# Performance work log

Hardware: AMD Instinct MI355X
Metric: run time of the kernel (lower is better)

## Reference

```python
import jax, jax.numpy as jnp
import numpy as np

DT_SCALER = 1.0 / 24.0
ODE_STEPS = 4  # fixed-step RK4 stand-in for adaptive odeint(rtol=atol=1e-3)
B, T, D, H = 1024, 100, 32, 256
ODE_MID = 50  # hidden width of the ODE func MLP (hard-coded 50 in source)


def setup_inputs() -> dict:
    key = jax.random.key(0)
    ks = jax.random.split(key, 20)
    n = lambda k, s: jax.random.normal(k, s, dtype=jnp.float32)
    std = 0.1  # module inits weights N(0, 0.1), biases 0
    return {
        "dt": jax.random.uniform(ks[0], (B, T, 2), dtype=jnp.float32),
        "x": n(ks[1], (B, T, D)),
        # RNNCell params
        "W_ih": n(ks[2], (H, D)) * std,
        "b_ih": jnp.zeros((H,), jnp.float32),
        "W_hh": n(ks[3], (H, H)) * std,
        "b_hh": jnp.zeros((H,), jnp.float32),
        # ODE func: Linear(H,50) -> tanh -> Linear(50,H)
        "ode_w1": n(ks[4], (ODE_MID, H)) * std,
        "ode_b1": jnp.zeros((ODE_MID,), jnp.float32),
        "ode_w2": n(ks[5], (H, ODE_MID)) * std,
        "ode_b2": jnp.zeros((H,), jnp.float32),
        # mu head: l1 (H -> H//2), distribution_mu (H//2 -> 1)
        "l1_w": n(ks[6], (H // 2, H)) * std,
        "l1_b": jnp.zeros((H // 2,), jnp.float32),
        "mu_w": n(ks[7], (1, H // 2)) * std,
        "mu_b": jnp.zeros((1,), jnp.float32),
        # sigma head: Linear(H,H) -> tanh -> Linear(H,1) -> softplus
        "sig_w1": n(ks[8], (H, H)) * std,
        "sig_b1": jnp.zeros((H,), jnp.float32),
        "sig_w2": n(ks[9], (1, H)) * std,
        "sig_b2": jnp.zeros((1,), jnp.float32),
    }


def reference(dt, x, W_ih, b_ih, W_hh, b_hh, ode_w1, ode_b1, ode_w2, ode_b2,
              l1_w, l1_b, mu_w, mu_b, sig_w1, sig_b1, sig_w2, sig_b2):
    Bsz = x.shape[0]
    xs = jnp.swapaxes(x, 0, 1)                               # [T,B,D]
    dts = jnp.swapaxes(dt[:, :, 1] - dt[:, :, 0], 0, 1)[..., None]  # [T,B,1]
    h0 = jnp.zeros((Bsz, W_hh.shape[0]), x.dtype)
    hs = 1.0 / ODE_STEPS

    def ode_f(y, scale):
        # net(y) * (dt * DT_SCALER); RHS is time-independent
        return (jnp.tanh(y @ ode_w1.T + ode_b1) @ ode_w2.T + ode_b2) * scale

    def step(h, inp):
        x_i, dt_i = inp                                      # [B,D], [B,1]
        # h_t = h_t + RNNCell(x_i, h_t)
        h = h + jnp.tanh(x_i @ W_ih.T + b_ih + h @ W_hh.T + b_hh)
        scale = dt_i * DT_SCALER
        # integrate dh/dt = ode_f(h) from t=0 to t=1 (fixed-step RK4)
        def rk4(y, _):
            k1 = ode_f(y, scale)
            k2 = ode_f(y + 0.5 * hs * k1, scale)
            k3 = ode_f(y + 0.5 * hs * k2, scale)
            k4 = ode_f(y + hs * k3, scale)
            return y + (hs / 6.0) * (k1 + 2.0 * k2 + 2.0 * k3 + k4), None
        h, _ = jax.lax.scan(rk4, h, None, length=ODE_STEPS)
        # heads (eval mode: dropout is identity)
        mu = jax.nn.relu(h @ l1_w.T + l1_b) @ mu_w.T + mu_b              # [B,1]
        sig = jax.nn.softplus(jnp.tanh(h @ sig_w1.T + sig_b1) @ sig_w2.T + sig_b2)
        return h, (mu, sig)

    _, (mu_seq, sig_seq) = jax.lax.scan(step, h0, (xs, dts))
    mu_out = jnp.swapaxes(mu_seq, 0, 1)    # [B,T,1]
    sig_out = jnp.swapaxes(sig_seq, 0, 1)  # [B,T,1]
    return (mu_out, sig_out)
```

## Files before the change

### kernel.cpp

```cpp
#include <hip/hip_runtime.h>
#include <math.h>


#define NT 512

#define WS_WCAT 0
#define WS_L1P  73728
#define WS_SW1  106496
#define WS_TOT  172032

#define SM_PR1 0
#define SM_PR2 10240
#define SM_H   20480
#define SM_YC  21504
#define SM_AC  22528
#define SM_MD  23552
#define SM_X4  23808
#define SM_BC  23936
#define SM_OB1 24192
#define SM_OB2 24256
#define SM_L1B 24512
#define SM_SB1 24640
#define SM_MUW 24896
#define SM_SW2 25024
#define SM_SCL 25280
#define SM_TOT 25288
#define SMEM_BYTES (SM_TOT * 4)

__device__ __forceinline__ float fma4(float acc, float4 y, float4 w) {
  acc = fmaf(y.x, w.x, acc);
  acc = fmaf(y.y, w.y, acc);
  acc = fmaf(y.z, w.z, acc);
  acc = fmaf(y.w, w.w, acc);
  return acc;
}

__device__ __forceinline__ float4 add4(float4 a, float4 b) {
  return make_float4(a.x + b.x, a.y + b.y, a.z + b.z, a.w + b.w);
}

__device__ __forceinline__ float tfast(float x) {
  float ax = fabsf(x);
  float e  = __expf(-2.f * ax);
  float t  = (1.f - e) * __builtin_amdgcn_rcpf(1.f + e);
  return copysignf(t, x);
}

__device__ __forceinline__ float4 tfast4(float4 v) {
  return make_float4(tfast(v.x), tfast(v.y), tfast(v.z), tfast(v.w));
}

__global__ void prep_transpose(const float* __restrict__ Wih,
                               const float* __restrict__ Whh,
                               const float* __restrict__ l1w,
                               const float* __restrict__ sw1,
                               float* __restrict__ ws) {
  int i = blockIdx.x * 256 + threadIdx.x;
  if (i < 73728) {
    int g = i >> 10, rem = i & 1023, j = rem >> 2, c = rem & 3;
    int k = 4 * g + c;
    ws[i] = (k < 32) ? Wih[j * 32 + k] : Whh[j * 256 + (k - 32)];
  } else if (i < 106496) {
    int t = i - 73728;
    int g = t >> 9, rem = t & 511, j = rem >> 2, c = rem & 3;
    ws[i] = l1w[j * 256 + 4 * g + c];
  } else if (i < WS_TOT) {
    int t = i - 106496;
    int g = t >> 10, rem = t & 1023, j = rem >> 2, c = rem & 3;
    ws[i] = sw1[j * 256 + 4 * g + c];
  }
}

__global__ __attribute__((amdgpu_flat_work_group_size(NT, NT)))
__attribute__((amdgpu_waves_per_eu(2)))
void odernn_main(const float* __restrict__ dt,
                 const float* __restrict__ x,
                 const float* __restrict__ bih,
                 const float* __restrict__ bhh,
                 const float* __restrict__ ow1,
                 const float* __restrict__ ob1g,
                 const float* __restrict__ ow2,
                 const float* __restrict__ ob2g,
                 const float* __restrict__ l1bg,
                 const float* __restrict__ muwg,
                 const float* __restrict__ mubg,
                 const float* __restrict__ sb1g,
                 const float* __restrict__ sw2g,
                 const float* __restrict__ sb2g,
                 const float* __restrict__ ws,
                 float* __restrict__ out) {
  extern __shared__ __align__(16) float sm[];
  const int tid = threadIdx.x;
  const int wv = tid >> 6, ln = tid & 63;
  const int b0 = blockIdx.x * 4;

  float* prS  = sm + SM_PR1;
  float* prS2 = sm + SM_PR2;
  float* hS   = sm + SM_H;
  float* ycS  = sm + SM_YC;
  float* acS  = sm + SM_AC;
  float* mdS  = sm + SM_MD;
  float* x4S  = sm + SM_X4;
  float* bcS  = sm + SM_BC;
  float* ob1S = sm + SM_OB1;
  float* ob2S = sm + SM_OB2;
  float* l1bS = sm + SM_L1B;
  float* sb1S = sm + SM_SB1;
  float* muwS = sm + SM_MUW;
  float* sw2S = sm + SM_SW2;
  float* sclS = sm + SM_SCL;

  float4* pr1_4 = (float4*)prS;
  float4* pr2_4 = (float4*)prS2;
  float4* h4   = (float4*)hS;
  float4* yc4  = (float4*)ycS;
  float4* ac4  = (float4*)acS;
  float4* md4w = (float4*)mdS;
  float4* l1o4 = (float4*)ycS;
  float4* sg4  = (float4*)acS;
  const float4* h44  = (const float4*)hS;
  const float4* yc44 = (const float4*)ycS;
  const float4* md4  = (const float4*)mdS;
  const float4* x44  = (const float4*)x4S;
  const float4* bc4  = (const float4*)bcS;
  const float4* ob1_4 = (const float4*)ob1S;
  const float4* ob2_4 = (const float4*)ob2S;
  const float4* l1b4 = (const float4*)l1bS;
  const float4* sb14 = (const float4*)sb1S;
  const float4* muw4 = (const float4*)muwS;
  const float4* sw24 = (const float4*)sw2S;

  const float4* wcat4 = (const float4*)(ws + WS_WCAT);
  const float4* l1w4  = (const float4*)(ws + WS_L1P);
  const float4* sw14  = (const float4*)(ws + WS_SW1);

  const int q1 = tid & 15, kc1 = tid >> 4;
  const int cq2 = tid & 63, kc2 = tid >> 6;
  float4 w1r[4][2];
  float4 w2r[4][2];
  {
#pragma unroll
    for (int n = 0; n < 4; ++n) {
      int row = 4 * q1 + n;
#pragma unroll
      for (int g = 0; g < 2; ++g) {
        if (row < 50)
          w1r[n][g] = *(const float4*)&ow1[row * 256 + kc1 * 8 + 4 * g];
        else
          w1r[n][g] = make_float4(0.f, 0.f, 0.f, 0.f);
      }
    }
    float w2tmp[4];
#pragma unroll
    for (int n = 0; n < 4; ++n) {
      int col = 4 * cq2 + n;
#pragma unroll
      for (int g = 0; g < 2; ++g) {
#pragma unroll
        for (int c = 0; c < 4; ++c) {
          int k = kc2 * 8 + 4 * g + c;
          w2tmp[c] = (k < 50) ? ow2[col * 50 + k] : 0.f;
        }
        w2r[n][g] = make_float4(w2tmp[0], w2tmp[1], w2tmp[2], w2tmp[3]);
      }
    }
  }

  if (tid < 256) {
    bcS[tid]  = bih[tid] + bhh[tid];
    ob2S[tid] = ob2g[tid];
    sb1S[tid] = sb1g[tid];
    sw2S[tid] = sw2g[tid];
  }
  if (tid < 64)  ob1S[tid] = (tid < 50) ? ob1g[tid] : 0.f;
  if (tid < 128) { l1bS[tid] = l1bg[tid]; muwS[tid] = muwg[tid]; }
  hS[tid] = 0.f; hS[tid + 512] = 0.f;
  __syncthreads();

  const float mub = mubg[0], sb2 = sb2g[0];

  for (int t = 0; t < 100; ++t) {
    if (tid < 128) {
      int r = tid >> 5, kk = tid & 31;
      x4S[r * 32 + kk] = x[((size_t)(b0 + r) * 100 + t) * 32 + kk];
    }
    if (tid < 4) {
      const float* dp = dt + ((size_t)(b0 + tid) * 100 + t) * 2;
      sclS[tid] = (dp[1] - dp[0]) * (1.f / 24.f);
    }
    __syncthreads();

    {
      const int jq = tid & 63, kc = tid >> 6;
      float4 acc0 = make_float4(0, 0, 0, 0), acc1 = acc0, acc2 = acc0, acc3 = acc0;
#pragma unroll 3
      for (int gg = 0; gg < 9; ++gg) {
        int g = kc * 9 + gg;
        float4 w0 = wcat4[g * 256 + 4 * jq + 0];
        float4 w1 = wcat4[g * 256 + 4 * jq + 1];
        float4 w2 = wcat4[g * 256 + 4 * jq + 2];
        float4 w3 = wcat4[g * 256 + 4 * jq + 3];
        float4 y0 = (g < 8) ? x44[0 * 8 + g] : h44[0 * 64 + (g - 8)];
        float4 y1 = (g < 8) ? x44[1 * 8 + g] : h44[1 * 64 + (g - 8)];
        float4 y2 = (g < 8) ? x44[2 * 8 + g] : h44[2 * 64 + (g - 8)];
        float4 y3 = (g < 8) ? x44[3 * 8 + g] : h44[3 * 64 + (g - 8)];
        acc0.x = fma4(acc0.x, y0, w0); acc0.y = fma4(acc0.y, y0, w1);
        acc0.z = fma4(acc0.z, y0, w2); acc0.w = fma4(acc0.w, y0, w3);
        acc1.x = fma4(acc1.x, y1, w0); acc1.y = fma4(acc1.y, y1, w1);
        acc1.z = fma4(acc1.z, y1, w2); acc1.w = fma4(acc1.w, y1, w3);
        acc2.x = fma4(acc2.x, y2, w0); acc2.y = fma4(acc2.y, y2, w1);
        acc2.z = fma4(acc2.z, y2, w2); acc2.w = fma4(acc2.w, y2, w3);
        acc3.x = fma4(acc3.x, y3, w0); acc3.y = fma4(acc3.y, y3, w1);
        acc3.z = fma4(acc3.z, y3, w2); acc3.w = fma4(acc3.w, y3, w3);
      }
      pr1_4[tid * 5 + 0] = acc0;
      pr1_4[tid * 5 + 1] = acc1;
      pr1_4[tid * 5 + 2] = acc2;
      pr1_4[tid * 5 + 3] = acc3;
    }
    __syncthreads();
    if (tid < 256) {
      const int r = tid >> 6, jq = tid & 63;
      const float4* base = pr1_4 + (jq * 5 + r);
      float4 v = base[0];
#pragma unroll
      for (int kc = 1; kc < 8; ++kc) v = add4(v, base[kc * 320]);
      v = add4(v, bc4[jq]);
      int o4 = r * 64 + jq;
      h4[o4] = add4(h4[o4], tfast4(v));
    }
    __syncthreads();

#pragma unroll 1
    for (int os = 0; os < 4; ++os) {
#pragma unroll
      for (int s = 0; s < 4; ++s) {
        {
          const float4* ysrc = (s == 0) ? h44 : yc44;
          float4 a0 = make_float4(0, 0, 0, 0), a1 = a0, a2 = a0, a3 = a0;
#pragma unroll
          for (int g = 0; g < 2; ++g) {
            float4 y0 = ysrc[0 * 64 + kc1 * 2 + g];
            float4 y1 = ysrc[1 * 64 + kc1 * 2 + g];
            float4 y2 = ysrc[2 * 64 + kc1 * 2 + g];
            float4 y3 = ysrc[3 * 64 + kc1 * 2 + g];
            a0.x = fma4(a0.x, y0, w1r[0][g]); a0.y = fma4(a0.y, y0, w1r[1][g]);
            a0.z = fma4(a0.z, y0, w1r[2][g]); a0.w = fma4(a0.w, y0, w1r[3][g]);
            a1.x = fma4(a1.x, y1, w1r[0][g]); a1.y = fma4(a1.y, y1, w1r[1][g]);
            a1.z = fma4(a1.z, y1, w1r[2][g]); a1.w = fma4(a1.w, y1, w1r[3][g]);
            a2.x = fma4(a2.x, y2, w1r[0][g]); a2.y = fma4(a2.y, y2, w1r[1][g]);
            a2.z = fma4(a2.z, y2, w1r[2][g]); a2.w = fma4(a2.w, y2, w1r[3][g]);
            a3.x = fma4(a3.x, y3, w1r[0][g]); a3.y = fma4(a3.y, y3, w1r[1][g]);
            a3.z = fma4(a3.z, y3, w1r[2][g]); a3.w = fma4(a3.w, y3, w1r[3][g]);
          }
          pr1_4[tid * 5 + 0] = a0;
          pr1_4[tid * 5 + 1] = a1;
          pr1_4[tid * 5 + 2] = a2;
          pr1_4[tid * 5 + 3] = a3;
        }
        __syncthreads();
        if (tid < 256) {
          const int r = tid >> 6, qr = (tid >> 2) & 15, sub = tid & 3;
          const float4* base = pr1_4 + ((sub * 16 + qr) * 5 + r);
          float4 v = base[0];
#pragma unroll
          for (int i = 1; i < 8; ++i) v = add4(v, base[i * 320]);
          v.x += __shfl_xor(v.x, 1); v.y += __shfl_xor(v.y, 1);
          v.z += __shfl_xor(v.z, 1); v.w += __shfl_xor(v.w, 1);
          v.x += __shfl_xor(v.x, 2); v.y += __shfl_xor(v.y, 2);
          v.z += __shfl_xor(v.z, 2); v.w += __shfl_xor(v.w, 2);
          if (sub == 0)
            md4w[r * 16 + qr] = tfast4(add4(v, ob1_4[qr]));
        }
        __syncthreads();
        {
          float4 b0v = make_float4(0, 0, 0, 0), b1v = b0v, b2v = b0v, b3v = b0v;
#pragma unroll
          for (int g = 0; g < 2; ++g) {
            float4 m0 = md4[0 * 16 + kc2 * 2 + g];
            float4 m1 = md4[1 * 16 + kc2 * 2 + g];
            float4 m2 = md4[2 * 16 + kc2 * 2 + g];
            float4 m3 = md4[3 * 16 + kc2 * 2 + g];
            b0v.x = fma4(b0v.x, m0, w2r[0][g]); b0v.y = fma4(b0v.y, m0, w2r[1][g]);
            b0v.z = fma4(b0v.z, m0, w2r[2][g]); b0v.w = fma4(b0v.w, m0, w2r[3][g]);
            b1v.x = fma4(b1v.x, m1, w2r[0][g]); b1v.y = fma4(b1v.y, m1, w2r[1][g]);
            b1v.z = fma4(b1v.z, m1, w2r[2][g]); b1v.w = fma4(b1v.w, m1, w2r[3][g]);
            b2v.x = fma4(b2v.x, m2, w2r[0][g]); b2v.y = fma4(b2v.y, m2, w2r[1][g]);
            b2v.z = fma4(b2v.z, m2, w2r[2][g]); b2v.w = fma4(b2v.w, m2, w2r[3][g]);
            b3v.x = fma4(b3v.x, m3, w2r[0][g]); b3v.y = fma4(b3v.y, m3, w2r[1][g]);
            b3v.z = fma4(b3v.z, m3, w2r[2][g]); b3v.w = fma4(b3v.w, m3, w2r[3][g]);
          }
          pr2_4[tid * 5 + 0] = b0v;
          pr2_4[tid * 5 + 1] = b1v;
          pr2_4[tid * 5 + 2] = b2v;
          pr2_4[tid * 5 + 3] = b3v;
        }
        __syncthreads();
        if (tid < 256) {
          const int r = tid >> 6, cq = tid & 63;
          const float4* base = pr2_4 + (cq * 5 + r);
          float4 v = base[0];
#pragma unroll
          for (int kc = 1; kc < 8; ++kc) v = add4(v, base[kc * 320]);
          v = add4(v, ob2_4[cq]);
          float sc = sclS[r];
          float4 kv = make_float4(v.x * sc, v.y * sc, v.z * sc, v.w * sc);
          int o4 = r * 64 + cq;
          if (s == 0) {
            ac4[o4] = kv;
            float4 hv = h4[o4];
            yc4[o4] = make_float4(hv.x + 0.125f * kv.x, hv.y + 0.125f * kv.y,
                                  hv.z + 0.125f * kv.z, hv.w + 0.125f * kv.w);
          } else if (s == 1) {
            float4 a = ac4[o4];
            ac4[o4] = make_float4(a.x + 2.f * kv.x, a.y + 2.f * kv.y,
                                  a.z + 2.f * kv.z, a.w + 2.f * kv.w);
            float4 hv = h4[o4];
            yc4[o4] = make_float4(hv.x + 0.125f * kv.x, hv.y + 0.125f * kv.y,
                                  hv.z + 0.125f * kv.z, hv.w + 0.125f * kv.w);
          } else if (s == 2) {
            float4 a = ac4[o4];
            ac4[o4] = make_float4(a.x + 2.f * kv.x, a.y + 2.f * kv.y,
                                  a.z + 2.f * kv.z, a.w + 2.f * kv.w);
            float4 hv = h4[o4];
            yc4[o4] = make_float4(hv.x + 0.25f * kv.x, hv.y + 0.25f * kv.y,
                                  hv.z + 0.25f * kv.z, hv.w + 0.25f * kv.w);
          } else {
            float4 a = ac4[o4];
            float4 hv = h4[o4];
            const float c6 = 0.25f / 6.f;
            h4[o4] = make_float4(hv.x + c6 * (a.x + kv.x), hv.y + c6 * (a.y + kv.y),
                                 hv.z + c6 * (a.z + kv.z), hv.w + c6 * (a.w + kv.w));
          }
        }
        __syncthreads();
      }
    }

    {
      const int cq = tid & 31, kc = tid >> 5;
      float4 c0 = make_float4(0, 0, 0, 0), c1 = c0, c2 = c0, c3 = c0;
#pragma unroll 2
      for (int g = 0; g < 4; ++g) {
        int kg = kc * 4 + g;
        float4 w0 = l1w4[kg * 128 + 4 * cq + 0];
        float4 w1 = l1w4[kg * 128 + 4 * cq + 1];
        float4 w2 = l1w4[kg * 128 + 4 * cq + 2];
        float4 w3 = l1w4[kg * 128 + 4 * cq + 3];
        float4 y0 = h44[0 * 64 + kg], y1 = h44[1 * 64 + kg];
        float4 y2 = h44[2 * 64 + kg], y3 = h44[3 * 64 + kg];
        c0.x = fma4(c0.x, y0, w0); c0.y = fma4(c0.y, y0, w1);
        c0.z = fma4(c0.z, y0, w2); c0.w = fma4(c0.w, y0, w3);
        c1.x = fma4(c1.x, y1, w0); c1.y = fma4(c1.y, y1, w1);
        c1.z = fma4(c1.z, y1, w2); c1.w = fma4(c1.w, y1, w3);
        c2.x = fma4(c2.x, y2, w0); c2.y = fma4(c2.y, y2, w1);
        c2.z = fma4(c2.z, y2, w2); c2.w = fma4(c2.w, y2, w3);
        c3.x = fma4(c3.x, y3, w0); c3.y = fma4(c3.y, y3, w1);
        c3.z = fma4(c3.z, y3, w2); c3.w = fma4(c3.w, y3, w3);
      }
      pr1_4[tid * 5 + 0] = c0;
      pr1_4[tid * 5 + 1] = c1;
      pr1_4[tid * 5 + 2] = c2;
      pr1_4[tid * 5 + 3] = c3;
    }
    {
      const int cq = tid & 63, kc = tid >> 6;
      float4 d0 = make_float4(0, 0, 0, 0), d1 = d0, d2 = d0, d3 = d0;
#pragma unroll 2
      for (int g = 0; g < 8; ++g) {
        int kg = kc * 8 + g;
        float4 w0 = sw14[kg * 256 + 4 * cq + 0];
        float4 w1 = sw14[kg * 256 + 4 * cq + 1];
        float4 w2 = sw14[kg * 256 + 4 * cq + 2];
        float4 w3 = sw14[kg * 256 + 4 * cq + 3];
        float4 y0 = h44[0 * 64 + kg], y1 = h44[1 * 64 + kg];
        float4 y2 = h44[2 * 64 + kg], y3 = h44[3 * 64 + kg];
        d0.x = fma4(d0.x, y0, w0); d0.y = fma4(d0.y, y0, w1);
        d0.z = fma4(d0.z, y0, w2); d0.w = fma4(d0.w, y0, w3);
        d1.x = fma4(d1.x, y1, w0); d1.y = fma4(d1.y, y1, w1);
        d1.z = fma4(d1.z, y1, w2); d1.w = fma4(d1.w, y1, w3);
        d2.x = fma4(d2.x, y2, w0); d2.y = fma4(d2.y, y2, w1);
        d2.z = fma4(d2.z, y2, w2); d2.w = fma4(d2.w, y2, w3);
        d3.x = fma4(d3.x, y3, w0); d3.y = fma4(d3.y, y3, w1);
        d3.z = fma4(d3.z, y3, w2); d3.w = fma4(d3.w, y3, w3);
      }
      pr2_4[tid * 5 + 0] = d0;
      pr2_4[tid * 5 + 1] = d1;
      pr2_4[tid * 5 + 2] = d2;
      pr2_4[tid * 5 + 3] = d3;
    }
    __syncthreads();
    if (tid < 256) {
      const int outQ = tid >> 1, sub = tid & 1;
      const int r = outQ >> 5, cq = outQ & 31;
      const float4* base = pr1_4 + ((sub * 32 + cq) * 5 + r);
      float4 v = base[0];
#pragma unroll
      for (int i = 1; i < 8; ++i) v = add4(v, base[i * 320]);
      v.x += __shfl_xor(v.x, 1); v.y += __shfl_xor(v.y, 1);
      v.z += __shfl_xor(v.z, 1); v.w += __shfl_xor(v.w, 1);
      if (sub == 0) {
        float4 b = l1b4[cq];
        l1o4[r * 32 + cq] = make_float4(fmaxf(v.x + b.x, 0.f), fmaxf(v.y + b.y, 0.f),
                                        fmaxf(v.z + b.z, 0.f), fmaxf(v.w + b.w, 0.f));
      }
    } else {
      const int t2 = tid & 255;
      const int r = t2 >> 6, cq = t2 & 63;
      const float4* base = pr2_4 + (cq * 5 + r);
      float4 v = base[0];
#pragma unroll
      for (int kc = 1; kc < 8; ++kc) v = add4(v, base[kc * 320]);
      sg4[r * 64 + cq] = tfast4(add4(v, sb14[cq]));
    }
    __syncthreads();
    {
      if (wv < 4) {
        const int r = wv, c = ln & 31;
        float4 l = l1o4[r * 32 + c], w = muw4[c];
        float pm = (ln < 32) ? (l.x * w.x + l.y * w.y + l.z * w.z + l.w * w.w) : 0.f;
#pragma unroll
        for (int off = 32; off > 0; off >>= 1) pm += __shfl_down(pm, off);
        if (ln == 0) out[(size_t)(b0 + r) * 100 + t] = pm + mub;
      } else {
        const int r = wv - 4;
        float4 s4 = sg4[r * 64 + ln], w = sw24[ln];
        float ps = s4.x * w.x + s4.y * w.y + s4.z * w.z + s4.w * w.w;
#pragma unroll
        for (int off = 32; off > 0; off >>= 1) ps += __shfl_down(ps, off);
        if (ln == 0) {
          float z = ps + sb2;
          float sp = fmaxf(z, 0.f) + log1pf(expf(-fabsf(z)));
          out[(size_t)102400 + (size_t)(b0 + r) * 100 + t] = sp;
        }
      }
    }
  }
}

extern "C" void kernel_launch(void* const* d_in, const int* in_sizes, int n_in,
                              void* d_out, int out_size, void* d_ws, size_t ws_size,
                              hipStream_t stream) {
  const float* dt  = (const float*)d_in[0];
  const float* x   = (const float*)d_in[1];
  const float* Wih = (const float*)d_in[2];
  const float* bih = (const float*)d_in[3];
  const float* Whh = (const float*)d_in[4];
  const float* bhh = (const float*)d_in[5];
  const float* ow1 = (const float*)d_in[6];
  const float* ob1 = (const float*)d_in[7];
  const float* ow2 = (const float*)d_in[8];
  const float* ob2 = (const float*)d_in[9];
  const float* l1w = (const float*)d_in[10];
  const float* l1b = (const float*)d_in[11];
  const float* muw = (const float*)d_in[12];
  const float* mub = (const float*)d_in[13];
  const float* sw1 = (const float*)d_in[14];
  const float* sb1 = (const float*)d_in[15];
  const float* sw2 = (const float*)d_in[16];
  const float* sb2 = (const float*)d_in[17];
  float* ws  = (float*)d_ws;
  float* out = (float*)d_out;

  hipFuncSetAttribute((const void*)odernn_main,
                      hipFuncAttributeMaxDynamicSharedMemorySize, SMEM_BYTES);

  prep_transpose<<<WS_TOT / 256, 256, 0, stream>>>(Wih, Whh, l1w, sw1, ws);
  odernn_main<<<256, NT, SMEM_BYTES, stream>>>(dt, x, bih, bhh, ow1, ob1, ow2, ob2,
                                               l1b, muw, mub, sb1, sw2, sb2, ws, out);
}
```

Measured before the change: 3.846 ms.

## Halve batch rows per block to double grid size and raise occupancy

Each workgroup now processes 2 batch rows instead of 4, so the grid grows from 256 to 512 blocks, filling more of the GPU's compute units. Partial-sum buffers are re-laid out into a single compact region with new reduction indexing and cross-lane shuffles, which shrinks LDS use, and the waves-per-EU hint rises to 4. The trade-off is that each weight load from global/L2 is now reused across only 2 rows instead of 4, doubling total weight traffic per step, and the recurrent time loop stays just as serial with the same number of barriers.

```diff
diff --git a/kernel.cpp b/kernel.cpp
--- a/kernel.cpp
+++ b/kernel.cpp
@@ -9,22 +9,21 @@
 #define WS_SW1  106496
 #define WS_TOT  172032
 
-#define SM_PR1 0
-#define SM_PR2 10240
-#define SM_H   20480
-#define SM_YC  21504
-#define SM_AC  22528
-#define SM_MD  23552
-#define SM_X4  23808
-#define SM_BC  23936
-#define SM_OB1 24192
-#define SM_OB2 24256
-#define SM_L1B 24512
-#define SM_SB1 24640
-#define SM_MUW 24896
-#define SM_SW2 25024
-#define SM_SCL 25280
-#define SM_TOT 25288
+#define SM_PR  0
+#define SM_H   8192
+#define SM_YC  8704
+#define SM_AC  9216
+#define SM_MD  9728
+#define SM_X4  9856
+#define SM_BC  9920
+#define SM_OB1 10176
+#define SM_OB2 10240
+#define SM_L1B 10496
+#define SM_SB1 10624
+#define SM_MUW 10880
+#define SM_SW2 11008
+#define SM_SCL 11264
+#define SM_TOT 11272
 #define SMEM_BYTES (SM_TOT * 4)
 
 __device__ __forceinline__ float fma4(float acc, float4 y, float4 w) {
@@ -72,7 +71,7 @@
 }
 
 __global__ __attribute__((amdgpu_flat_work_group_size(NT, NT)))
-__attribute__((amdgpu_waves_per_eu(2)))
+__attribute__((amdgpu_waves_per_eu(4)))
 void odernn_main(const float* __restrict__ dt,
                  const float* __restrict__ x,
                  const float* __restrict__ bih,
@@ -92,14 +91,9 @@
   extern __shared__ __align__(16) float sm[];
   const int tid = threadIdx.x;
   const int wv = tid >> 6, ln = tid & 63;
-  const int b0 = blockIdx.x * 4;
-
-  float* prS  = sm + SM_PR1;
-  float* prS2 = sm + SM_PR2;
+  const int b0 = blockIdx.x * 2;
+
   float* hS   = sm + SM_H;
-  float* ycS  = sm + SM_YC;
-  float* acS  = sm + SM_AC;
-  float* mdS  = sm + SM_MD;
   float* x4S  = sm + SM_X4;
   float* bcS  = sm + SM_BC;
   float* ob1S = sm + SM_OB1;
@@ -110,18 +104,17 @@
   float* sw2S = sm + SM_SW2;
   float* sclS = sm + SM_SCL;
 
-  float4* pr1_4 = (float4*)prS;
-  float4* pr2_4 = (float4*)prS2;
-  float4* h4   = (float4*)hS;
-  float4* yc4  = (float4*)ycS;
-  float4* ac4  = (float4*)acS;
-  float4* md4w = (float4*)mdS;
-  float4* l1o4 = (float4*)ycS;
-  float4* sg4  = (float4*)acS;
-  const float4* h44  = (const float4*)hS;
-  const float4* yc44 = (const float4*)ycS;
-  const float4* md4  = (const float4*)mdS;
-  const float4* x44  = (const float4*)x4S;
+  float4* pr4  = (float4*)(sm + SM_PR);
+  float4* h4   = (float4*)(sm + SM_H);
+  float4* yc4  = (float4*)(sm + SM_YC);
+  float4* ac4  = (float4*)(sm + SM_AC);
+  float4* md4w = (float4*)(sm + SM_MD);
+  float4* l1o4 = (float4*)(sm + SM_YC);
+  float4* sg4  = (float4*)(sm + SM_AC);
+  const float4* h44  = (const float4*)(sm + SM_H);
+  const float4* yc44 = (const float4*)(sm + SM_YC);
+  const float4* md4  = (const float4*)(sm + SM_MD);
+  const float4* x44  = (const float4*)(sm + SM_X4);
   const float4* bc4  = (const float4*)bcS;
   const float4* ob1_4 = (const float4*)ob1S;
   const float4* ob2_4 = (const float4*)ob2S;
@@ -174,17 +167,17 @@
   }
   if (tid < 64)  ob1S[tid] = (tid < 50) ? ob1g[tid] : 0.f;
   if (tid < 128) { l1bS[tid] = l1bg[tid]; muwS[tid] = muwg[tid]; }
-  hS[tid] = 0.f; hS[tid + 512] = 0.f;
+  if (tid < 512) hS[tid] = 0.f;
   __syncthreads();
 
   const float mub = mubg[0], sb2 = sb2g[0];
 
   for (int t = 0; t < 100; ++t) {
-    if (tid < 128) {
+    if (tid < 64) {
       int r = tid >> 5, kk = tid & 31;
       x4S[r * 32 + kk] = x[((size_t)(b0 + r) * 100 + t) * 32 + kk];
     }
-    if (tid < 4) {
+    if (tid < 2) {
       const float* dp = dt + ((size_t)(b0 + tid) * 100 + t) * 2;
       sclS[tid] = (dp[1] - dp[0]) * (1.f / 24.f);
     }
@@ -192,7 +185,7 @@
 
     {
       const int jq = tid & 63, kc = tid >> 6;
-      float4 acc0 = make_float4(0, 0, 0, 0), acc1 = acc0, acc2 = acc0, acc3 = acc0;
+      float4 acc0 = make_float4(0, 0, 0, 0), acc1 = acc0;
 #pragma unroll 3
       for (int gg = 0; gg < 9; ++gg) {
         int g = kc * 9 + gg;
@@ -200,31 +193,22 @@
         float4 w1 = wcat4[g * 256 + 4 * jq + 1];
         float4 w2 = wcat4[g * 256 + 4 * jq + 2];
         float4 w3 = wcat4[g * 256 + 4 * jq + 3];
-        float4 y0 = (g < 8) ? x44[0 * 8 + g] : h44[0 * 64 + (g - 8)];
-        float4 y1 = (g < 8) ? x44[1 * 8 + g] : h44[1 * 64 + (g - 8)];
-        float4 y2 = (g < 8) ? x44[2 * 8 + g] : h44[2 * 64 + (g - 8)];
-        float4 y3 = (g < 8) ? x44[3 * 8 + g] : h44[3 * 64 + (g - 8)];
+        float4 y0 = (g < 8) ? x44[g]     : h44[g - 8];
+        float4 y1 = (g < 8) ? x44[8 + g] : h44[64 + (g - 8)];
         acc0.x = fma4(acc0.x, y0, w0); acc0.y = fma4(acc0.y, y0, w1);
         acc0.z = fma4(acc0.z, y0, w2); acc0.w = fma4(acc0.w, y0, w3);
         acc1.x = fma4(acc1.x, y1, w0); acc1.y = fma4(acc1.y, y1, w1);
         acc1.z = fma4(acc1.z, y1, w2); acc1.w = fma4(acc1.w, y1, w3);
-        acc2.x = fma4(acc2.x, y2, w0); acc2.y = fma4(acc2.y, y2, w1);
-        acc2.z = fma4(acc2.z, y2, w2); acc2.w = fma4(acc2.w, y2, w3);
-        acc3.x = fma4(acc3.x, y3, w0); acc3.y = fma4(acc3.y, y3, w1);
-        acc3.z = fma4(acc3.z, y3, w2); acc3.w = fma4(acc3.w, y3, w3);
-      }
-      pr1_4[tid * 5 + 0] = acc0;
-      pr1_4[tid * 5 + 1] = acc1;
-      pr1_4[tid * 5 + 2] = acc2;
-      pr1_4[tid * 5 + 3] = acc3;
+      }
+      pr4[(kc * 2 + 0) * 64 + jq] = acc0;
+      pr4[(kc * 2 + 1) * 64 + jq] = acc1;
     }
     __syncthreads();
-    if (tid < 256) {
+    if (tid < 128) {
       const int r = tid >> 6, jq = tid & 63;
-      const float4* base = pr1_4 + (jq * 5 + r);
-      float4 v = base[0];
-#pragma unroll
-      for (int kc = 1; kc < 8; ++kc) v = add4(v, base[kc * 320]);
+      float4 v = pr4[r * 64 + jq];
+#pragma unroll
+      for (int kc = 1; kc < 8; ++kc) v = add4(v, pr4[(kc * 2 + r) * 64 + jq]);
       v = add4(v, bc4[jq]);
       int o4 = r * 64 + jq;
       h4[o4] = add4(h4[o4], tfast4(v));
@@ -237,71 +221,54 @@
       for (int s = 0; s < 4; ++s) {
         {
           const float4* ysrc = (s == 0) ? h44 : yc44;
-          float4 a0 = make_float4(0, 0, 0, 0), a1 = a0, a2 = a0, a3 = a0;
+          float4 a0 = make_float4(0, 0, 0, 0), a1 = a0;
 #pragma unroll
           for (int g = 0; g < 2; ++g) {
-            float4 y0 = ysrc[0 * 64 + kc1 * 2 + g];
-            float4 y1 = ysrc[1 * 64 + kc1 * 2 + g];
-            float4 y2 = ysrc[2 * 64 + kc1 * 2 + g];
-            float4 y3 = ysrc[3 * 64 + kc1 * 2 + g];
+            float4 y0 = ysrc[kc1 * 2 + g];
+            float4 y1 = ysrc[64 + kc1 * 2 + g];
             a0.x = fma4(a0.x, y0, w1r[0][g]); a0.y = fma4(a0.y, y0, w1r[1][g]);
             a0.z = fma4(a0.z, y0, w1r[2][g]); a0.w = fma4(a0.w, y0, w1r[3][g]);
             a1.x = fma4(a1.x, y1, w1r[0][g]); a1.y = fma4(a1.y, y1, w1r[1][g]);
             a1.z = fma4(a1.z, y1, w1r[2][g]); a1.w = fma4(a1.w, y1, w1r[3][g]);
-            a2.x = fma4(a2.x, y2, w1r[0][g]); a2.y = fma4(a2.y, y2, w1r[1][g]);
-            a2.z = fma4(a2.z, y2, w1r[2][g]); a2.w = fma4(a2.w, y2, w1r[3][g]);
-            a3.x = fma4(a3.x, y3, w1r[0][g]); a3.y = fma4(a3.y, y3, w1r[1][g]);
-            a3.z = fma4(a3.z, y3, w1r[2][g]); a3.w = fma4(a3.w, y3, w1r[3][g]);
           }
-          pr1_4[tid * 5 + 0] = a0;
-          pr1_4[tid * 5 + 1] = a1;
-          pr1_4[tid * 5 + 2] = a2;
-          pr1_4[tid * 5 + 3] = a3;
+          pr4[(kc1 * 2 + 0) * 16 + q1] = a0;
+          pr4[(kc1 * 2 + 1) * 16 + q1] = a1;
         }
         __syncthreads();
-        if (tid < 256) {
-          const int r = tid >> 6, qr = (tid >> 2) & 15, sub = tid & 3;
-          const float4* base = pr1_4 + ((sub * 16 + qr) * 5 + r);
-          float4 v = base[0];
-#pragma unroll
-          for (int i = 1; i < 8; ++i) v = add4(v, base[i * 320]);
-          v.x += __shfl_xor(v.x, 1); v.y += __shfl_xor(v.y, 1);
-          v.z += __shfl_xor(v.z, 1); v.w += __shfl_xor(v.w, 1);
-          v.x += __shfl_xor(v.x, 2); v.y += __shfl_xor(v.y, 2);
-          v.z += __shfl_xor(v.z, 2); v.w += __shfl_xor(v.w, 2);
+        if (tid < 128) {
+          const int r = tid >> 6, sub = (tid >> 4) & 3, qq = tid & 15;
+          float4 v = pr4[(sub * 8 * 2 + r) * 16 + qq];
+#pragma unroll
+          for (int i = 1; i < 8; ++i)
+            v = add4(v, pr4[((sub * 8 + i) * 2 + r) * 16 + qq]);
+          v.x += __shfl_xor(v.x, 16); v.y += __shfl_xor(v.y, 16);
+          v.z += __shfl_xor(v.z, 16); v.w += __shfl_xor(v.w, 16);
+          v.x += __shfl_xor(v.x, 32); v.y += __shfl_xor(v.y, 32);
+          v.z += __shfl_xor(v.z, 32); v.w += __shfl_xor(v.w, 32);
           if (sub == 0)
-            md4w[r * 16 + qr] = tfast4(add4(v, ob1_4[qr]));
+            md4w[r * 16 + qq] = tfast4(add4(v, ob1_4[qq]));
         }
         __syncthreads();
         {
-          float4 b0v = make_float4(0, 0, 0, 0), b1v = b0v, b2v = b0v, b3v = b0v;
+          float4 b0v = make_float4(0, 0, 0, 0), b1v = b0v;
 #pragma unroll
           for (int g = 0; g < 2; ++g) {
-            float4 m0 = md4[0 * 16 + kc2 * 2 + g];
-            float4 m1 = md4[1 * 16 + kc2 * 2 + g];
-            float4 m2 = md4[2 * 16 + kc2 * 2 + g];
-            float4 m3 = md4[3 * 16 + kc2 * 2 + g];
+            float4 m0 = md4[kc2 * 2 + g];
+            float4 m1 = md4[16 + kc2 * 2 + g];
             b0v.x = fma4(b0v.x, m0, w2r[0][g]); b0v.y = fma4(b0v.y, m0, w2r[1][g]);
             b0v.z = fma4(b0v.z, m0, w2r[2][g]); b0v.w = fma4(b0v.w, m0, w2r[3][g]);
             b1v.x = fma4(b1v.x, m1, w2r[0][g]); b1v.y = fma4(b1v.y, m1, w2r[1][g]);
             b1v.z = fma4(b1v.z, m1, w2r[2][g]); b1v.w = fma4(b1v.w, m1, w2r[3][g]);
-            b2v.x = fma4(b2v.x, m2, w2r[0][g]); b2v.y = fma4(b2v.y, m2, w2r[1][g]);
-            b2v.z = fma4(b2v.z, m2, w2r[2][g]); b2v.w = fma4(b2v.w, m2, w2r[3][g]);
-            b3v.x = fma4(b3v.x, m3, w2r[0][g]); b3v.y = fma4(b3v.y, m3, w2r[1][g]);
-            b3v.z = fma4(b3v.z, m3, w2r[2][g]); b3v.w = fma4(b3v.w, m3, w2r[3][g]);
           }
-          pr2_4[tid * 5 + 0] = b0v;
-          pr2_4[tid * 5 + 1] = b1v;
-          pr2_4[tid * 5 + 2] = b2v;
-          pr2_4[tid * 5 + 3] = b3v;
+          pr4[(kc2 * 2 + 0) * 64 + cq2] = b0v;
+          pr4[(kc2 * 2 + 1) * 64 + cq2] = b1v;
         }
         __syncthreads();
-        if (tid < 256) {
+        if (tid < 128) {
           const int r = tid >> 6, cq = tid & 63;
-          const float4* base = pr2_4 + (cq * 5 + r);
-          float4 v = base[0];
-#pragma unroll
-          for (int kc = 1; kc < 8; ++kc) v = add4(v, base[kc * 320]);
+          float4 v = pr4[r * 64 + cq];
+#pragma unroll
+          for (int kc = 1; kc < 8; ++kc) v = add4(v, pr4[(kc * 2 + r) * 64 + cq]);
           v = add4(v, ob2_4[cq]);
           float sc = sclS[r];
           float4 kv = make_float4(v.x * sc, v.y * sc, v.z * sc, v.w * sc);
@@ -339,7 +306,7 @@
 
     {
       const int cq = tid & 31, kc = tid >> 5;
-      float4 c0 = make_float4(0, 0, 0, 0), c1 = c0, c2 = c0, c3 = c0;
+      float4 c0 = make_float4(0, 0, 0, 0), c1 = c0;
 #pragma unroll 2
       for (int g = 0; g < 4; ++g) {
         int kg = kc * 4 + g;
@@ -347,92 +314,74 @@
         float4 w1 = l1w4[kg * 128 + 4 * cq + 1];
         float4 w2 = l1w4[kg * 128 + 4 * cq + 2];
         float4 w3 = l1w4[kg * 128 + 4 * cq + 3];
-        float4 y0 = h44[0 * 64 + kg], y1 = h44[1 * 64 + kg];
-        float4 y2 = h44[2 * 64 + kg], y3 = h44[3 * 64 + kg];
+        float4 y0 = h44[kg], y1 = h44[64 + kg];
         c0.x = fma4(c0.x, y0, w0); c0.y = fma4(c0.y, y0, w1);
         c0.z = fma4(c0.z, y0, w2); c0.w = fma4(c0.w, y0, w3);
         c1.x = fma4(c1.x, y1, w0); c1.y = fma4(c1.y, y1, w1);
         c1.z = fma4(c1.z, y1, w2); c1.w = fma4(c1.w, y1, w3);
-        c2.x = fma4(c2.x, y2, w0); c2.y = fma4(c2.y, y2, w1);
-        c2.z = fma4(c2.z, y2, w2); c2.w = fma4(c2.w, y2, w3);
-        c3.x = fma4(c3.x, y3, w0); c3.y = fma4(c3.y, y3, w1);
-        c3.z = fma4(c3.z, y3, w2); c3.w = fma4(c3.w, y3, w3);
-      }
-      pr1_4[tid * 5 + 0] = c0;
-      pr1_4[tid * 5 + 1] = c1;
-      pr1_4[tid * 5 + 2] = c2;
-      pr1_4[tid * 5 + 3] = c3;
+      }
+      pr4[(kc * 2 + 0) * 32 + cq] = c0;
+      pr4[(kc * 2 + 1) * 32 + cq] = c1;
     }
     {
-      const int cq = tid & 63, kc = tid >> 6;
-      float4 d0 = make_float4(0, 0, 0, 0), d1 = d0, d2 = d0, d3 = d0;
+      float4 d0 = make_float4(0, 0, 0, 0), d1 = d0;
 #pragma unroll 2
       for (int g = 0; g < 8; ++g) {
-        int kg = kc * 8 + g;
-        float4 w0 = sw14[kg * 256 + 4 * cq + 0];
-        float4 w1 = sw14[kg * 256 + 4 * cq + 1];
-        float4 w2 = sw14[kg * 256 + 4 * cq + 2];
-        float4 w3 = sw14[kg * 256 + 4 * cq + 3];
-        float4 y0 = h44[0 * 64 + kg], y1 = h44[1 * 64 + kg];
-        float4 y2 = h44[2 * 64 + kg], y3 = h44[3 * 64 + kg];
+        int kg = kc2 * 8 + g;
+        float4 w0 = sw14[kg * 256 + 4 * cq2 + 0];
+        float4 w1 = sw14[kg * 256 + 4 * cq2 + 1];
+        float4 w2 = sw14[kg * 256 + 4 * cq2 + 2];
+        float4 w3 = sw14[kg * 256 + 4 * cq2 + 3];
+        float4 y0 = h44[kg], y1 = h44[64 + kg];
         d0.x = fma4(d0.x, y0, w0); d0.y = fma4(d0.y, y0, w1);
         d0.z = fma4(d0.z, y0, w2); d0.w = fma4(d0.w, y0, w3);
         d1.x = fma4(d1.x, y1, w0); d1.y = fma4(d1.y, y1, w1);
         d1.z = fma4(d1.z, y1, w2); d1.w = fma4(d1.w, y1, w3);
-        d2.x = fma4(d2.x, y2, w0); d2.y = fma4(d2.y, y2, w1);
-        d2.z = fma4(d2.z, y2, w2); d2.w = fma4(d2.w, y2, w3);
-        d3.x = fma4(d3.x, y3, w0); d3.y = fma4(d3.y, y3, w1);
-        d3.z = fma4(d3.z, y3, w2); d3.w = fma4(d3.w, y3, w3);
-      }
-      pr2_4[tid * 5 + 0] = d0;
-      pr2_4[tid * 5 + 1] = d1;
-      pr2_4[tid * 5 + 2] = d2;
-      pr2_4[tid * 5 + 3] = d3;
+      }
+      pr4[1024 + (kc2 * 2 + 0) * 64 + cq2] = d0;
+      pr4[1024 + (kc2 * 2 + 1) * 64 + cq2] = d1;
     }
     __syncthreads();
-    if (tid < 256) {
-      const int outQ = tid >> 1, sub = tid & 1;
-      const int r = outQ >> 5, cq = outQ & 31;
-      const float4* base = pr1_4 + ((sub * 32 + cq) * 5 + r);
-      float4 v = base[0];
-#pragma unroll
-      for (int i = 1; i < 8; ++i) v = add4(v, base[i * 320]);
-      v.x += __shfl_xor(v.x, 1); v.y += __shfl_xor(v.y, 1);
-      v.z += __shfl_xor(v.z, 1); v.w += __shfl_xor(v.w, 1);
+    if (tid < 128) {
+      const int r = tid >> 6, sub = (tid >> 5) & 1, cq = tid & 31;
+      float4 v = pr4[(sub * 8 * 2 + r) * 32 + cq];
+#pragma unroll
+      for (int i = 1; i < 8; ++i)
+        v = add4(v, pr4[((sub * 8 + i) * 2 + r) * 32 + cq]);
+      v.x += __shfl_xor(v.x, 32); v.y += __shfl_xor(v.y, 32);
+      v.z += __shfl_xor(v.z, 32); v.w += __shfl_xor(v.w, 32);
       if (sub == 0) {
         float4 b = l1b4[cq];
         l1o4[r * 32 + cq] = make_float4(fmaxf(v.x + b.x, 0.f), fmaxf(v.y + b.y, 0.f),
                                         fmaxf(v.z + b.z, 0.f), fmaxf(v.w + b.w, 0.f));
       }
-    } else {
-      const int t2 = tid & 255;
+    } else if (tid < 256) {
+      const int t2 = tid - 128;
       const int r = t2 >> 6, cq = t2 & 63;
-      const float4* base = pr2_4 + (cq * 5 + r);
-      float4 v = base[0];
-#pragma unroll
-      for (int kc = 1; kc < 8; ++kc) v = add4(v, base[kc * 320]);
+      float4 v = pr4[1024 + r * 64 + cq];
+#pragma unroll
+      for (int kc = 1; kc < 8; ++kc)
+        v = add4(v, pr4[1024 + (kc * 2 + r) * 64 + cq]);
       sg4[r * 64 + cq] = tfast4(add4(v, sb14[cq]));
     }
     __syncthreads();
-    {
-      if (wv < 4) {
-        const int r = wv, c = ln & 31;
-        float4 l = l1o4[r * 32 + c], w = muw4[c];
-        float pm = (ln < 32) ? (l.x * w.x + l.y * w.y + l.z * w.z + l.w * w.w) : 0.f;
-#pragma unroll
-        for (int off = 32; off > 0; off >>= 1) pm += __shfl_down(pm, off);
-        if (ln == 0) out[(size_t)(b0 + r) * 100 + t] = pm + mub;
-      } else {
-        const int r = wv - 4;
-        float4 s4 = sg4[r * 64 + ln], w = sw24[ln];
-        float ps = s4.x * w.x + s4.y * w.y + s4.z * w.z + s4.w * w.w;
-#pragma unroll
-        for (int off = 32; off > 0; off >>= 1) ps += __shfl_down(ps, off);
-        if (ln == 0) {
-          float z = ps + sb2;
-          float sp = fmaxf(z, 0.f) + log1pf(expf(-fabsf(z)));
-          out[(size_t)102400 + (size_t)(b0 + r) * 100 + t] = sp;
-        }
+    if (wv < 2) {
+      const int r = wv, c = ln & 31;
+      float4 l = l1o4[r * 32 + c], w = muw4[c];
+      float pm = (ln < 32) ? (l.x * w.x + l.y * w.y + l.z * w.z + l.w * w.w) : 0.f;
+#pragma unroll
+      for (int off = 32; off > 0; off >>= 1) pm += __shfl_down(pm, off);
+      if (ln == 0) out[(size_t)(b0 + r) * 100 + t] = pm + mub;
+    } else if (wv < 4) {
+      const int r = wv - 2;
+      float4 s4 = sg4[r * 64 + ln], w = sw24[ln];
+      float ps = s4.x * w.x + s4.y * w.y + s4.z * w.z + s4.w * w.w;
+#pragma unroll
+      for (int off = 32; off > 0; off >>= 1) ps += __shfl_down(ps, off);
+      if (ln == 0) {
+        float z = ps + sb2;
+        float sp = fmaxf(z, 0.f) + log1pf(expf(-fabsf(z)));
+        out[(size_t)102400 + (size_t)(b0 + r) * 100 + t] = sp;
       }
     }
   }
@@ -466,6 +415,6 @@
                       hipFuncAttributeMaxDynamicSharedMemorySize, SMEM_BYTES);
 
   prep_transpose<<<WS_TOT / 256, 256, 0, stream>>>(Wih, Whh, l1w, sw1, ws);
-  odernn_main<<<256, NT, SMEM_BYTES, stream>>>(dt, x, bih, bhh, ow1, ob1, ow2, ob2,
+  odernn_main<<<512, NT, SMEM_BYTES, stream>>>(dt, x, bih, bhh, ow1, ob1, ow2, ob2,
                                                l1b, muw, mub, sb1, sw2, sb2, ws, out);
 }
```

Measured after the change: 3.755 ms. 2.4% less time.
